# Performance work log

Hardware: AMD Instinct MI355X
Metric: run time of the kernel (lower is better)

The kernel has to match this reference:

```python
import jax, jax.numpy as jnp
import numpy as np

N_NODES = 100000
N_EDGES = 1600000
IN_F = 64
HIDDEN = [64, 64, 32]


def _glorot(key, shape):
    limit = float(np.sqrt(6.0 / (shape[0] + shape[1])))
    return jax.random.uniform(key, shape, jnp.float32, -limit, limit)


def setup_inputs() -> dict:
    key = jax.random.key(0)
    ks = jax.random.split(key, 5)
    x = jax.random.normal(ks[0], (N_NODES, IN_F), jnp.float32)
    edge_index = jax.random.randint(ks[1], (2, N_EDGES), 0, N_NODES, jnp.int64)
    dims = [IN_F] + HIDDEN
    params = {}
    for i in range(len(HIDDEN)):
        params[f"W{i+1}"] = _glorot(ks[2 + i], (dims[i], dims[i + 1]))
        params[f"b{i+1}"] = jnp.zeros((dims[i + 1],), jnp.float32)
    return {"x": x, "edge_index": edge_index, **params}


def _gcn_layer(x, src, dst, norm, W, b, n):
    # PyG GCNConv: linear transform, then normalized scatter-sum aggregation, then bias
    h = x @ W                                  # [N, out]
    msg = norm[:, None] * h[src]               # gather + edge scaling, [E+N, out]
    out = jax.ops.segment_sum(msg, dst, num_segments=n)
    return out + b


def reference(x, edge_index, W1, b1, W2, b2, W3, b3):
    n = x.shape[0]
    # add self-loops (GCNConv default add_self_loops=True)
    loops = jnp.arange(n, dtype=edge_index.dtype)
    src = jnp.concatenate([edge_index[0], loops])
    dst = jnp.concatenate([edge_index[1], loops])
    # symmetric normalization: deg over destination (col), norm = d^-1/2[src]*d^-1/2[dst]
    deg = jax.ops.segment_sum(jnp.ones_like(src, x.dtype), dst, num_segments=n)
    dinv = jnp.where(deg > 0, jax.lax.rsqrt(deg), 0.0)
    norm = dinv[src] * dinv[dst]
    h = jax.nn.relu(_gcn_layer(x, src, dst, norm, W1, b1, n))
    h = jax.nn.relu(_gcn_layer(h, src, dst, norm, W2, b2, n))
    return _gcn_layer(h, src, dst, norm, W3, b3, n)
```

## Files before the change

kernel.cpp:

```cpp
#include <hip/hip_runtime.h>
#include <hip/hip_bf16.h>


#define BLOCK 256
#define NBUCKET 512
#define CHUNK 4096
#define SLOT 4608
#define MAX_NPB 256

typedef float f32x4 __attribute__((ext_vector_type(4)));
typedef short bf16x8 __attribute__((ext_vector_type(8)));

__device__ __forceinline__ unsigned int bf16r(float f) {
  unsigned int u = __float_as_uint(f);
  u += 0x7fffu + ((u >> 16) & 1u);
  return u >> 16;
}

__device__ __forceinline__ void bsplit(float v, unsigned int& h,
                                       unsigned int& l) {
  h = bf16r(v);
  float r = v - __uint_as_float(h << 16);
  l = bf16r(r);
}

__device__ __forceinline__ void acc_bf8(float4& lo, float4& hi, uint4 u) {
  lo.x += __uint_as_float(u.x << 16);
  lo.y += __uint_as_float(u.x & 0xffff0000u);
  lo.z += __uint_as_float(u.y << 16);
  lo.w += __uint_as_float(u.y & 0xffff0000u);
  hi.x += __uint_as_float(u.z << 16);
  hi.y += __uint_as_float(u.z & 0xffff0000u);
  hi.z += __uint_as_float(u.w << 16);
  hi.w += __uint_as_float(u.w & 0xffff0000u);
}


__global__ __launch_bounds__(BLOCK) void binning_kernel(
    const int* __restrict__ src, const int* __restrict__ dst,
    int* __restrict__ bcursor, int* __restrict__ binned, int e, int npb) {
  __shared__ int h[NBUCKET];
  __shared__ int base[NBUCKET];
  for (int i = threadIdx.x; i < NBUCKET; i += BLOCK) h[i] = 0;
  __syncthreads();
  const int cbase = blockIdx.x * CHUNK;
#pragma unroll
  for (int k = 0; k < CHUNK; k += BLOCK * 4) {
    int i = cbase + k + threadIdx.x * 4;
    if (i + 3 < e) {
      int4 d4 = *(const int4*)(dst + i);
      atomicAdd(&h[d4.x / npb], 1);
      atomicAdd(&h[d4.y / npb], 1);
      atomicAdd(&h[d4.z / npb], 1);
      atomicAdd(&h[d4.w / npb], 1);
    } else {
      for (int t = 0; t < 4; ++t)
        if (i + t < e) atomicAdd(&h[dst[i + t] / npb], 1);
    }
  }
  __syncthreads();
  for (int i = threadIdx.x; i < NBUCKET; i += BLOCK) {
    int c = h[i];
    base[i] = c ? atomicAdd(&bcursor[i], c) : 0;
    h[i] = 0;
  }
  __syncthreads();
#pragma unroll
  for (int k = 0; k < CHUNK; k += BLOCK * 4) {
    int i = cbase + k + threadIdx.x * 4;
    if (i + 3 < e) {
      int4 d4 = *(const int4*)(dst + i);
      int4 s4 = *(const int4*)(src + i);
      int b0 = d4.x / npb, b1 = d4.y / npb, b2 = d4.z / npb, b3 = d4.w / npb;
      int o0 = atomicAdd(&h[b0], 1);
      int o1 = atomicAdd(&h[b1], 1);
      int o2 = atomicAdd(&h[b2], 1);
      int o3 = atomicAdd(&h[b3], 1);
      binned[b0 * SLOT + base[b0] + o0] = s4.x | ((d4.x - b0 * npb) << 17);
      binned[b1 * SLOT + base[b1] + o1] = s4.y | ((d4.y - b1 * npb) << 17);
      binned[b2 * SLOT + base[b2] + o2] = s4.z | ((d4.z - b2 * npb) << 17);
      binned[b3 * SLOT + base[b3] + o3] = s4.w | ((d4.w - b3 * npb) << 17);
    } else {
      for (int t = 0; t < 4; ++t) {
        if (i + t < e) {
          int d = dst[i + t];
          int bkt = d / npb;
          int lofs = atomicAdd(&h[bkt], 1);
          binned[bkt * SLOT + base[bkt] + lofs] =
              src[i + t] | ((d - bkt * npb) << 17);
        }
      }
    }
  }
}

__global__ __launch_bounds__(BLOCK) void bucket_build(
    const int* __restrict__ binned, const int* __restrict__ bcursor,
    int* __restrict__ offs, int* __restrict__ cnt, float* __restrict__ dinv,
    int* __restrict__ csr_src, int n, int npb) {
  __shared__ int nhist[MAX_NPB];
  __shared__ int noff[MAX_NPB];
  __shared__ int lcsr[SLOT];
  __shared__ int ptot_sh;
  const int b = blockIdx.x;
  const int node_base = b * npb;
  const int nodes = min(npb, n - node_base);
  if (nodes <= 0) return;
  const int ebase = b * SLOT;
  const int ecnt = bcursor[b];
  for (int i = threadIdx.x; i < npb; i += BLOCK) nhist[i] = 0;
  __syncthreads();
  for (int i = threadIdx.x; i < ecnt; i += BLOCK)
    atomicAdd(&nhist[binned[ebase + i] >> 17], 1);
  __syncthreads();
  if (threadIdx.x < 64) {
    const int lane = threadIdx.x;
    const int bi = lane * 4;
    int v0 = (bi + 0 < nodes) ? nhist[bi + 0] : 0;
    int v1 = (bi + 1 < nodes) ? nhist[bi + 1] : 0;
    int v2 = (bi + 2 < nodes) ? nhist[bi + 2] : 0;
    int v3 = (bi + 3 < nodes) ? nhist[bi + 3] : 0;
    int p0 = (v0 + 3) & ~3;
    int p1 = (v1 + 3) & ~3;
    int p2 = (v2 + 3) & ~3;
    int p3 = (v3 + 3) & ~3;
    int tsum = p0 + p1 + p2 + p3;
    int s = tsum;
#pragma unroll
    for (int o = 1; o < 64; o <<= 1) {
      int u = __shfl_up(s, o, 64);
      if (lane >= o) s += u;
    }
    int texcl = s - tsum;
    if (bi + 0 < nodes) noff[bi + 0] = texcl;
    if (bi + 1 < nodes) noff[bi + 1] = texcl + p0;
    if (bi + 2 < nodes) noff[bi + 2] = texcl + p0 + p1;
    if (bi + 3 < nodes) noff[bi + 3] = texcl + p0 + p1 + p2;
    if (lane == 63) ptot_sh = s;
  }
  __syncthreads();
  const int ptot = min(ptot_sh, SLOT);
  for (int i = threadIdx.x; i < nodes; i += BLOCK) {
    int c = nhist[i];
    offs[node_base + i] = ebase + noff[i];
    cnt[node_base + i] = c;
    dinv[node_base + i] = rsqrtf((float)(c + 1));
  }
  for (int i = threadIdx.x; i < ptot; i += BLOCK) lcsr[i] = n;
  __syncthreads();
  for (int i = threadIdx.x; i < ecnt; i += BLOCK) {
    int v = binned[ebase + i];
    int pos = atomicAdd(&noff[v >> 17], 1);
    lcsr[pos] = v & 0x1ffff;
  }
  __syncthreads();
  for (int i = threadIdx.x; i < ptot; i += BLOCK)
    csr_src[ebase + i] = lcsr[i];
}

__global__ __launch_bounds__(BLOCK) void wprep_kernel(
    const float* __restrict__ W1, const float* __restrict__ W2,
    const float* __restrict__ W3, unsigned short* __restrict__ Wt) {
  int t = blockIdx.x * BLOCK + threadIdx.x;
  float v;
  int hi_off, lo_off;
  if (t < 4096) {
    int nn = t >> 6, k = t & 63;
    v = W1[k * 64 + nn];
    hi_off = t;
    lo_off = 4096 + t;
  } else if (t < 8192) {
    int i = t - 4096;
    int nn = i >> 6, k = i & 63;
    v = W2[k * 64 + nn];
    hi_off = 8192 + i;
    lo_off = 12288 + i;
  } else {
    int i = t - 8192;
    if (i >= 2048) return;
    int nn = i >> 6, k = i & 63;
    v = W3[k * 32 + nn];
    hi_off = 16384 + i;
    lo_off = 18432 + i;
  }
  unsigned int h, l;
  bsplit(v, h, l);
  Wt[hi_off] = (unsigned short)h;
  Wt[lo_off] = (unsigned short)l;
}


__global__ __launch_bounds__(BLOCK) void gemm1_kernel(
    const float* __restrict__ x, const unsigned short* __restrict__ Wt,
    const float* __restrict__ dinv, unsigned short* __restrict__ hbf, int n) {
  __shared__ unsigned short Ahi[16][72];
  __shared__ unsigned short Alo[16][72];
  __shared__ float dvs[16];
  if (blockIdx.x == 0 && threadIdx.x < 8)
    *(uint4*)(hbf + (size_t)n * 64 + threadIdx.x * 8) =
        make_uint4(0u, 0u, 0u, 0u);
  const int r16 = threadIdx.x >> 4;
  const int c4 = (threadIdx.x & 15) * 4;
  const int node = blockIdx.x * 16 + r16;
  const int wv = threadIdx.x >> 6;
  const int fr = threadIdx.x & 15;
  const int fq = (threadIdx.x >> 4) & 3;
  const unsigned short* wb = Wt + ((wv * 16 + fr) * 64) + fq * 8;
  bf16x8 bh0 = *(const bf16x8*)(wb);
  bf16x8 bh1 = *(const bf16x8*)(wb + 32);
  bf16x8 bl0 = *(const bf16x8*)(wb + 4096);
  bf16x8 bl1 = *(const bf16x8*)(wb + 4096 + 32);
  uint2 ph = make_uint2(0u, 0u), pl = make_uint2(0u, 0u);
  if (node < n) {
    f32x4 xv =
        __builtin_nontemporal_load((const f32x4*)(x + (size_t)node * 64 + c4));
    unsigned int h0, l0, h1, l1, h2, l2, h3, l3;
    bsplit(xv.x, h0, l0);
    bsplit(xv.y, h1, l1);
    bsplit(xv.z, h2, l2);
    bsplit(xv.w, h3, l3);
    ph = make_uint2(h0 | (h1 << 16), h2 | (h3 << 16));
    pl = make_uint2(l0 | (l1 << 16), l2 | (l3 << 16));
  }
  *(uint2*)(&Ahi[r16][c4]) = ph;
  *(uint2*)(&Alo[r16][c4]) = pl;
  if ((threadIdx.x & 15) == 0) dvs[r16] = (node < n) ? dinv[node] : 0.f;
  __syncthreads();
  bf16x8 ah0 = *(const bf16x8*)(&Ahi[fr][fq * 8]);
  bf16x8 ah1 = *(const bf16x8*)(&Ahi[fr][fq * 8 + 32]);
  bf16x8 aL0 = *(const bf16x8*)(&Alo[fr][fq * 8]);
  bf16x8 aL1 = *(const bf16x8*)(&Alo[fr][fq * 8 + 32]);
  f32x4 acc = {0.f, 0.f, 0.f, 0.f};
  acc = __builtin_amdgcn_mfma_f32_16x16x32_bf16(ah0, bh0, acc, 0, 0, 0);
  acc = __builtin_amdgcn_mfma_f32_16x16x32_bf16(aL0, bh0, acc, 0, 0, 0);
  acc = __builtin_amdgcn_mfma_f32_16x16x32_bf16(ah0, bl0, acc, 0, 0, 0);
  acc = __builtin_amdgcn_mfma_f32_16x16x32_bf16(ah1, bh1, acc, 0, 0, 0);
  acc = __builtin_amdgcn_mfma_f32_16x16x32_bf16(aL1, bh1, acc, 0, 0, 0);
  acc = __builtin_amdgcn_mfma_f32_16x16x32_bf16(ah1, bl1, acc, 0, 0, 0);
  const int col = wv * 16 + fr;
#pragma unroll
  for (int j = 0; j < 4; ++j) {
    int row = fq * 4 + j;
    int nd = blockIdx.x * 16 + row;
    if (nd < n)
      hbf[(size_t)nd * 64 + col] = (unsigned short)bf16r(dvs[row] * acc[j]);
  }
}

__global__ __launch_bounds__(BLOCK) void fused_agg_gemm64(
    const unsigned short* __restrict__ hin, const int* __restrict__ csr_src,
    const int* __restrict__ offs, const int* __restrict__ cnt,
    const float* __restrict__ dinv, const float* __restrict__ bias,
    const unsigned short* __restrict__ Wt, unsigned short* __restrict__ hout,
    int n) {
  __shared__ unsigned short Ahi[16][72];
  __shared__ unsigned short Alo[16][72];
  __shared__ float dvs[16];
  if (blockIdx.x == 0 && threadIdx.x < 8)
    *(uint4*)(hout + (size_t)n * 64 + threadIdx.x * 8) =
        make_uint4(0u, 0u, 0u, 0u);
  const int g = threadIdx.x >> 4;
  const int lane16 = threadIdx.x & 15;
  const int colgrp = lane16 & 7;
  const int half = lane16 >> 3;
  const int c8 = colgrp * 8;
  const int node = blockIdx.x * 16 + g;
  const bool valid = node < n;
  float dnode = 0.f;
  uint4 qh = make_uint4(0u, 0u, 0u, 0u), ql = make_uint4(0u, 0u, 0u, 0u);
  const char* hbase = (const char*)hin + c8 * 2;
  if (valid) {
    const int start = offs[node];
    const int cn = cnt[node];
    const int* cp = csr_src + start;
    float4 l0 = make_float4(0.f, 0.f, 0.f, 0.f), h0 = l0;
    float4 l1 = l0, h1 = l0, l2 = l0, h2 = l0, l3 = l0, h3 = l0;
    if (half == 0)
      acc_bf8(l0, h0, *(const uint4*)(hbase + ((unsigned)node << 7)));
    int j = half * 4;
    for (; j + 8 < cn; j += 16) {
      int4 sv0 = *(const int4*)(cp + j);
      int4 sv1 = *(const int4*)(cp + j + 8);
      uint4 u0 = *(const uint4*)(hbase + ((unsigned)sv0.x << 7));
      uint4 u1 = *(const uint4*)(hbase + ((unsigned)sv0.y << 7));
      uint4 u2 = *(const uint4*)(hbase + ((unsigned)sv0.z << 7));
      uint4 u3 = *(const uint4*)(hbase + ((unsigned)sv0.w << 7));
      uint4 u4 = *(const uint4*)(hbase + ((unsigned)sv1.x << 7));
      uint4 u5 = *(const uint4*)(hbase + ((unsigned)sv1.y << 7));
      uint4 u6 = *(const uint4*)(hbase + ((unsigned)sv1.z << 7));
      uint4 u7 = *(const uint4*)(hbase + ((unsigned)sv1.w << 7));
      acc_bf8(l0, h0, u0);
      acc_bf8(l1, h1, u1);
      acc_bf8(l2, h2, u2);
      acc_bf8(l3, h3, u3);
      acc_bf8(l0, h0, u4);
      acc_bf8(l1, h1, u5);
      acc_bf8(l2, h2, u6);
      acc_bf8(l3, h3, u7);
    }
    if (j < cn) {
      int4 sv = *(const int4*)(cp + j);
      uint4 u0 = *(const uint4*)(hbase + ((unsigned)sv.x << 7));
      uint4 u1 = *(const uint4*)(hbase + ((unsigned)sv.y << 7));
      uint4 u2 = *(const uint4*)(hbase + ((unsigned)sv.z << 7));
      uint4 u3 = *(const uint4*)(hbase + ((unsigned)sv.w << 7));
      acc_bf8(l0, h0, u0);
      acc_bf8(l1, h1, u1);
      acc_bf8(l2, h2, u2);
      acc_bf8(l3, h3, u3);
    }
    float4 alo = make_float4((l0.x + l1.x) + (l2.x + l3.x),
                             (l0.y + l1.y) + (l2.y + l3.y),
                             (l0.z + l1.z) + (l2.z + l3.z),
                             (l0.w + l1.w) + (l2.w + l3.w));
    float4 ahi = make_float4((h0.x + h1.x) + (h2.x + h3.x),
                             (h0.y + h1.y) + (h2.y + h3.y),
                             (h0.z + h1.z) + (h2.z + h3.z),
                             (h0.w + h1.w) + (h2.w + h3.w));
    alo.x += __shfl_xor(alo.x, 8); alo.y += __shfl_xor(alo.y, 8);
    alo.z += __shfl_xor(alo.z, 8); alo.w += __shfl_xor(alo.w, 8);
    ahi.x += __shfl_xor(ahi.x, 8); ahi.y += __shfl_xor(ahi.y, 8);
    ahi.z += __shfl_xor(ahi.z, 8); ahi.w += __shfl_xor(ahi.w, 8);
    dnode = dinv[node];
    if (half == 0) {
      float4 b4l = *(const float4*)(bias + c8);
      float4 b4h = *(const float4*)(bias + c8 + 4);
      float v0 = fmaxf(fmaf(dnode, alo.x, b4l.x), 0.f);
      float v1 = fmaxf(fmaf(dnode, alo.y, b4l.y), 0.f);
      float v2 = fmaxf(fmaf(dnode, alo.z, b4l.z), 0.f);
      float v3 = fmaxf(fmaf(dnode, alo.w, b4l.w), 0.f);
      float v4 = fmaxf(fmaf(dnode, ahi.x, b4h.x), 0.f);
      float v5 = fmaxf(fmaf(dnode, ahi.y, b4h.y), 0.f);
      float v6 = fmaxf(fmaf(dnode, ahi.z, b4h.z), 0.f);
      float v7 = fmaxf(fmaf(dnode, ahi.w, b4h.w), 0.f);
      unsigned int h0u, l0u, h1u, l1u, h2u, l2u, h3u, l3u;
      unsigned int h4u, l4u, h5u, l5u, h6u, l6u, h7u, l7u;
      bsplit(v0, h0u, l0u); bsplit(v1, h1u, l1u);
      bsplit(v2, h2u, l2u); bsplit(v3, h3u, l3u);
      bsplit(v4, h4u, l4u); bsplit(v5, h5u, l5u);
      bsplit(v6, h6u, l6u); bsplit(v7, h7u, l7u);
      qh = make_uint4(h0u | (h1u << 16), h2u | (h3u << 16),
                      h4u | (h5u << 16), h6u | (h7u << 16));
      ql = make_uint4(l0u | (l1u << 16), l2u | (l3u << 16),
                      l4u | (l5u << 16), l6u | (l7u << 16));
    }
  }
  if (half == 0) {
    *(uint4*)(&Ahi[g][c8]) = qh;
    *(uint4*)(&Alo[g][c8]) = ql;
    if (lane16 == 0) dvs[g] = dnode;
  }
  const int wv = threadIdx.x >> 6;
  const int fr = threadIdx.x & 15;
  const int fq = (threadIdx.x >> 4) & 3;
  const unsigned short* wb = Wt + ((wv * 16 + fr) * 64) + fq * 8;
  bf16x8 bh0 = *(const bf16x8*)(wb);
  bf16x8 bh1 = *(const bf16x8*)(wb + 32);
  bf16x8 bl0 = *(const bf16x8*)(wb + 4096);
  bf16x8 bl1 = *(const bf16x8*)(wb + 4096 + 32);
  __syncthreads();
  bf16x8 ah0 = *(const bf16x8*)(&Ahi[fr][fq * 8]);
  bf16x8 ah1 = *(const bf16x8*)(&Ahi[fr][fq * 8 + 32]);
  bf16x8 aL0 = *(const bf16x8*)(&Alo[fr][fq * 8]);
  bf16x8 aL1 = *(const bf16x8*)(&Alo[fr][fq * 8 + 32]);
  f32x4 acc = {0.f, 0.f, 0.f, 0.f};
  acc = __builtin_amdgcn_mfma_f32_16x16x32_bf16(ah0, bh0, acc, 0, 0, 0);
  acc = __builtin_amdgcn_mfma_f32_16x16x32_bf16(aL0, bh0, acc, 0, 0, 0);
  acc = __builtin_amdgcn_mfma_f32_16x16x32_bf16(ah0, bl0, acc, 0, 0, 0);
  acc = __builtin_amdgcn_mfma_f32_16x16x32_bf16(ah1, bh1, acc, 0, 0, 0);
  acc = __builtin_amdgcn_mfma_f32_16x16x32_bf16(aL1, bh1, acc, 0, 0, 0);
  acc = __builtin_amdgcn_mfma_f32_16x16x32_bf16(ah1, bl1, acc, 0, 0, 0);
  const int col = wv * 16 + fr;
#pragma unroll
  for (int j = 0; j < 4; ++j) {
    int row = fq * 4 + j;
    int nd = blockIdx.x * 16 + row;
    if (nd < n)
      hout[(size_t)nd * 64 + col] = (unsigned short)bf16r(dvs[row] * acc[j]);
  }
}

__global__ __launch_bounds__(BLOCK) void fused_agg_gemm32(
    const unsigned short* __restrict__ hin, const int* __restrict__ csr_src,
    const int* __restrict__ offs, const int* __restrict__ cnt,
    const float* __restrict__ dinv, const float* __restrict__ bias,
    const unsigned short* __restrict__ Wt, unsigned short* __restrict__ hout,
    int n) {
  __shared__ unsigned short Ahi[32][72];
  __shared__ unsigned short Alo[32][72];
  __shared__ float dvs[32];
  if (blockIdx.x == 0 && threadIdx.x < 4)
    *(uint4*)(hout + (size_t)n * 32 + threadIdx.x * 8) =
        make_uint4(0u, 0u, 0u, 0u);
  const int g = threadIdx.x >> 3;
  const int lane8 = threadIdx.x & 7;
  const int c8 = lane8 * 8;
  const int node = blockIdx.x * 32 + g;
  const bool valid = node < n;
  float dnode = 0.f;
  uint4 qh = make_uint4(0u, 0u, 0u, 0u), ql = make_uint4(0u, 0u, 0u, 0u);
  const char* hbase = (const char*)hin + c8 * 2;
  if (valid) {
    const int start = offs[node];
    const int cn = cnt[node];
    const int* cp = csr_src + start;
    float4 l0 = make_float4(0.f, 0.f, 0.f, 0.f), h0 = l0;
    float4 l1 = l0, h1 = l0, l2 = l0, h2 = l0, l3 = l0, h3 = l0;
    acc_bf8(l0, h0, *(const uint4*)(hbase + ((unsigned)node << 7)));
    int j = 0;
    for (; j + 4 < cn; j += 8) {
      int4 sv0 = *(const int4*)(cp + j);
      int4 sv1 = *(const int4*)(cp + j + 4);
      uint4 u0 = *(const uint4*)(hbase + ((unsigned)sv0.x << 7));
      uint4 u1 = *(const uint4*)(hbase + ((unsigned)sv0.y << 7));
      uint4 u2 = *(const uint4*)(hbase + ((unsigned)sv0.z << 7));
      uint4 u3 = *(const uint4*)(hbase + ((unsigned)sv0.w << 7));
      uint4 u4 = *(const uint4*)(hbase + ((unsigned)sv1.x << 7));
      uint4 u5 = *(const uint4*)(hbase + ((unsigned)sv1.y << 7));
      uint4 u6 = *(const uint4*)(hbase + ((unsigned)sv1.z << 7));
      uint4 u7 = *(const uint4*)(hbase + ((unsigned)sv1.w << 7));
      acc_bf8(l0, h0, u0);
      acc_bf8(l1, h1, u1);
      acc_bf8(l2, h2, u2);
      acc_bf8(l3, h3, u3);
      acc_bf8(l0, h0, u4);
      acc_bf8(l1, h1, u5);
      acc_bf8(l2, h2, u6);
      acc_bf8(l3, h3, u7);
    }
    if (j < cn) {
      int4 sv = *(const int4*)(cp + j);
      uint4 u0 = *(const uint4*)(hbase + ((unsigned)sv.x << 7));
      uint4 u1 = *(const uint4*)(hbase + ((unsigned)sv.y << 7));
      uint4 u2 = *(const uint4*)(hbase + ((unsigned)sv.z << 7));
      uint4 u3 = *(const uint4*)(hbase + ((unsigned)sv.w << 7));
      acc_bf8(l0, h0, u0);
      acc_bf8(l1, h1, u1);
      acc_bf8(l2, h2, u2);
      acc_bf8(l3, h3, u3);
    }
    float4 alo = make_float4((l0.x + l1.x) + (l2.x + l3.x),
                             (l0.y + l1.y) + (l2.y + l3.y),
                             (l0.z + l1.z) + (l2.z + l3.z),
                             (l0.w + l1.w) + (l2.w + l3.w));
    float4 ahi = make_float4((h0.x + h1.x) + (h2.x + h3.x),
                             (h0.y + h1.y) + (h2.y + h3.y),
                             (h0.z + h1.z) + (h2.z + h3.z),
                             (h0.w + h1.w) + (h2.w + h3.w));
    dnode = dinv[node];
    float4 b4l = *(const float4*)(bias + c8);
    float4 b4h = *(const float4*)(bias + c8 + 4);
    float v0 = fmaxf(fmaf(dnode, alo.x, b4l.x), 0.f);
    float v1 = fmaxf(fmaf(dnode, alo.y, b4l.y), 0.f);
    float v2 = fmaxf(fmaf(dnode, alo.z, b4l.z), 0.f);
    float v3 = fmaxf(fmaf(dnode, alo.w, b4l.w), 0.f);
    float v4 = fmaxf(fmaf(dnode, ahi.x, b4h.x), 0.f);
    float v5 = fmaxf(fmaf(dnode, ahi.y, b4h.y), 0.f);
    float v6 = fmaxf(fmaf(dnode, ahi.z, b4h.z), 0.f);
    float v7 = fmaxf(fmaf(dnode, ahi.w, b4h.w), 0.f);
    unsigned int h0u, l0u, h1u, l1u, h2u, l2u, h3u, l3u;
    unsigned int h4u, l4u, h5u, l5u, h6u, l6u, h7u, l7u;
    bsplit(v0, h0u, l0u); bsplit(v1, h1u, l1u);
    bsplit(v2, h2u, l2u); bsplit(v3, h3u, l3u);
    bsplit(v4, h4u, l4u); bsplit(v5, h5u, l5u);
    bsplit(v6, h6u, l6u); bsplit(v7, h7u, l7u);
    qh = make_uint4(h0u | (h1u << 16), h2u | (h3u << 16),
                    h4u | (h5u << 16), h6u | (h7u << 16));
    ql = make_uint4(l0u | (l1u << 16), l2u | (l3u << 16),
                    l4u | (l5u << 16), l6u | (l7u << 16));
  }
  *(uint4*)(&Ahi[g][c8]) = qh;
  *(uint4*)(&Alo[g][c8]) = ql;
  if (lane8 == 0) dvs[g] = dnode;
  const int wv = threadIdx.x >> 6;
  const int mt = wv >> 1;
  const int nt = wv & 1;
  const int fr = threadIdx.x & 15;
  const int fq = (threadIdx.x >> 4) & 3;
  const unsigned short* wb = Wt + ((nt * 16 + fr) * 64) + fq * 8;
  bf16x8 bh0 = *(const bf16x8*)(wb);
  bf16x8 bh1 = *(const bf16x8*)(wb + 32);
  bf16x8 bl0 = *(const bf16x8*)(wb + 2048);
  bf16x8 bl1 = *(const bf16x8*)(wb + 2048 + 32);
  __syncthreads();
  bf16x8 ah0 = *(const bf16x8*)(&Ahi[mt * 16 + fr][fq * 8]);
  bf16x8 ah1 = *(const bf16x8*)(&Ahi[mt * 16 + fr][fq * 8 + 32]);
  bf16x8 aL0 = *(const bf16x8*)(&Alo[mt * 16 + fr][fq * 8]);
  bf16x8 aL1 = *(const bf16x8*)(&Alo[mt * 16 + fr][fq * 8 + 32]);
  f32x4 acc = {0.f, 0.f, 0.f, 0.f};
  acc = __builtin_amdgcn_mfma_f32_16x16x32_bf16(ah0, bh0, acc, 0, 0, 0);
  acc = __builtin_amdgcn_mfma_f32_16x16x32_bf16(aL0, bh0, acc, 0, 0, 0);
  acc = __builtin_amdgcn_mfma_f32_16x16x32_bf16(ah0, bl0, acc, 0, 0, 0);
  acc = __builtin_amdgcn_mfma_f32_16x16x32_bf16(ah1, bh1, acc, 0, 0, 0);
  acc = __builtin_amdgcn_mfma_f32_16x16x32_bf16(aL1, bh1, acc, 0, 0, 0);
  acc = __builtin_amdgcn_mfma_f32_16x16x32_bf16(ah1, bl1, acc, 0, 0, 0);
  const int col = nt * 16 + fr;
#pragma unroll
  for (int j = 0; j < 4; ++j) {
    int row = mt * 16 + fq * 4 + j;
    int nd = blockIdx.x * 32 + row;
    if (nd < n)
      hout[(size_t)nd * 32 + col] = (unsigned short)bf16r(dvs[row] * acc[j]);
  }
}

__global__ __launch_bounds__(BLOCK) void agg3_kernel(
    const unsigned short* __restrict__ hbf, const int* __restrict__ csr_src,
    const int* __restrict__ offs, const int* __restrict__ cnt,
    const float* __restrict__ dinv, const float* __restrict__ bias,
    float* __restrict__ out, int n) {
  constexpr int F = 32;
  const int node = blockIdx.x * 64 + (int)(threadIdx.x >> 2);
  const int c8 = (threadIdx.x & 3) * 8;
  if (node >= n) return;
  const int start = offs[node];
  const int cn = cnt[node];
  const int* cp = csr_src + start;
  const char* hbase = (const char*)hbf + c8 * 2;
  float4 l0 = make_float4(0.f, 0.f, 0.f, 0.f), h0 = l0;
  float4 l1 = l0, h1 = l0, l2 = l0, h2 = l0, l3 = l0, h3 = l0;
  acc_bf8(l0, h0, *(const uint4*)(hbase + ((unsigned)node << 6)));
  for (int j = 0; j < cn; j += 4) {
    int4 sv = *(const int4*)(cp + j);
    uint4 u0 = *(const uint4*)(hbase + ((unsigned)sv.x << 6));
    uint4 u1 = *(const uint4*)(hbase + ((unsigned)sv.y << 6));
    uint4 u2 = *(const uint4*)(hbase + ((unsigned)sv.z << 6));
    uint4 u3 = *(const uint4*)(hbase + ((unsigned)sv.w << 6));
    acc_bf8(l0, h0, u0);
    acc_bf8(l1, h1, u1);
    acc_bf8(l2, h2, u2);
    acc_bf8(l3, h3, u3);
  }
  float4 alo = make_float4((l0.x + l1.x) + (l2.x + l3.x),
                           (l0.y + l1.y) + (l2.y + l3.y),
                           (l0.z + l1.z) + (l2.z + l3.z),
                           (l0.w + l1.w) + (l2.w + l3.w));
  float4 ahi = make_float4((h0.x + h1.x) + (h2.x + h3.x),
                           (h0.y + h1.y) + (h2.y + h3.y),
                           (h0.z + h1.z) + (h2.z + h3.z),
                           (h0.w + h1.w) + (h2.w + h3.w));
  float d = dinv[node];
  float4 blo = *(const float4*)(bias + c8);
  float4 bhi = *(const float4*)(bias + c8 + 4);
  f32x4 vlo = {fmaf(d, alo.x, blo.x), fmaf(d, alo.y, blo.y),
               fmaf(d, alo.z, blo.z), fmaf(d, alo.w, blo.w)};
  f32x4 vhi = {fmaf(d, ahi.x, bhi.x), fmaf(d, ahi.y, bhi.y),
               fmaf(d, ahi.z, bhi.z), fmaf(d, ahi.w, bhi.w)};
  float* op = out + (size_t)node * F + c8;
  __builtin_nontemporal_store(vlo, (f32x4*)op);
  __builtin_nontemporal_store(vhi, (f32x4*)(op + 4));
}

static inline size_t align_up(size_t v, size_t a) { return (v + a - 1) & ~(a - 1); }

extern "C" void kernel_launch(void* const* d_in, const int* in_sizes, int n_in,
                              void* d_out, int out_size, void* d_ws, size_t ws_size,
                              hipStream_t stream) {
  const float* x = (const float*)d_in[0];
  const int* edge_index = (const int*)d_in[1];
  const float* W1 = (const float*)d_in[2];
  const float* b1 = (const float*)d_in[3];
  const float* W2 = (const float*)d_in[4];
  const float* b2 = (const float*)d_in[5];
  const float* W3 = (const float*)d_in[6];
  const float* b3 = (const float*)d_in[7];
  float* out = (float*)d_out;

  const int n = in_sizes[0] / 64;
  const int e = in_sizes[1] / 2;
  const int* e_src = edge_index;
  const int* e_dst = edge_index + e;
  const int npb = (n + NBUCKET - 1) / NBUCKET;

  char* ws = (char*)d_ws;
  size_t off = 0;
  int* bcursor = (int*)(ws + off); off = align_up(off + NBUCKET * 4, 512);
  int* offs    = (int*)(ws + off); off = align_up(off + (size_t)n * 4, 512);
  int* cnt     = (int*)(ws + off); off = align_up(off + (size_t)n * 4, 512);
  float* dinv  = (float*)(ws + off); off = align_up(off + (size_t)n * 4, 512);
  int* binned  = (int*)(ws + off); off = align_up(off + (size_t)NBUCKET * SLOT * 4, 512);
  int* csr_src = (int*)(ws + off); off = align_up(off + (size_t)NBUCKET * SLOT * 4, 512);
  unsigned short* hbuf_a = (unsigned short*)(ws + off);
  off = align_up(off + (size_t)(n + 1) * 64 * 2, 512);
  unsigned short* hbuf_b = (unsigned short*)(ws + off);
  off = align_up(off + (size_t)(n + 1) * 64 * 2, 512);
  unsigned short* Wt = (unsigned short*)(ws + off);
  off = align_up(off + (size_t)20480 * 2, 512);
  (void)ws_size;

  unsigned short* Wt1 = Wt;
  unsigned short* Wt2 = Wt + 8192;
  unsigned short* Wt3 = Wt + 16384;

  const int gC = (e + CHUNK - 1) / CHUNK;

  hipMemsetAsync(bcursor, 0, NBUCKET * 4, stream);
  wprep_kernel<<<40, BLOCK, 0, stream>>>(W1, W2, W3, Wt);
  binning_kernel<<<gC, BLOCK, 0, stream>>>(e_src, e_dst, bcursor, binned, e, npb);
  bucket_build<<<NBUCKET, BLOCK, 0, stream>>>(binned, bcursor, offs, cnt, dinv,
                                              csr_src, n, npb);

  gemm1_kernel<<<(n + 15) / 16, BLOCK, 0, stream>>>(x, Wt1, dinv, hbuf_a, n);
  fused_agg_gemm64<<<(n + 15) / 16, BLOCK, 0, stream>>>(
      hbuf_a, csr_src, offs, cnt, dinv, b1, Wt2, hbuf_b, n);
  fused_agg_gemm32<<<(n + 31) / 32, BLOCK, 0, stream>>>(
      hbuf_b, csr_src, offs, cnt, dinv, b2, Wt3, hbuf_a, n);
  agg3_kernel<<<(n + 63) / 64, BLOCK, 0, stream>>>(hbuf_a, csr_src, offs, cnt,
                                                   dinv, b3, out, n);
}
```

Before: 237.3 us.

## Fold weight prep into binning, scatter CSR directly, unroll agg3 loop

The weight bf16 split/transpose moves into the binning kernel, which removes one kernel launch. bucket_build now writes CSR entries straight to global memory with per-node padding instead of staging them in a shared buffer, which cuts shared memory and two sync phases. The final aggregation loop is unrolled to 8 neighbours per iteration to keep more gathers in flight. The trade-off is scattered global writes in bucket_build and a small amount of extra work in binning blocks.

```diff
diff --git a/kernel.cpp b/kernel.cpp
--- a/kernel.cpp
+++ b/kernel.cpp
@@ -38,7 +38,47 @@
 
 __global__ __launch_bounds__(BLOCK) void binning_kernel(
     const int* __restrict__ src, const int* __restrict__ dst,
-    int* __restrict__ bcursor, int* __restrict__ binned, int e, int npb) {
+    int* __restrict__ bcursor, int* __restrict__ binned,
+    const float* __restrict__ W1, const float* __restrict__ W2,
+    const float* __restrict__ W3, unsigned short* __restrict__ Wt, int e,
+    int npb) {
+  {
+    int t = blockIdx.x * BLOCK + threadIdx.x;
+    if (t < 20480) {
+      float v;
+      int hi_off, lo_off;
+      if (t < 4096) {
+        int nn = t >> 6, k = t & 63;
+        v = W1[k * 64 + nn];
+        hi_off = t;
+        lo_off = 4096 + t;
+      } else if (t < 8192) {
+        int i = t - 4096;
+        int nn = i >> 6, k = i & 63;
+        v = W2[k * 64 + nn];
+        hi_off = 8192 + i;
+        lo_off = 12288 + i;
+      } else {
+        int i = t - 8192;
+        if (i < 2048) {
+          int nn = i >> 6, k = i & 63;
+          v = W3[k * 32 + nn];
+          hi_off = 16384 + i;
+          lo_off = 18432 + i;
+        } else {
+          hi_off = -1;
+          lo_off = -1;
+          v = 0.f;
+        }
+      }
+      if (hi_off >= 0) {
+        unsigned int h, l;
+        bsplit(v, h, l);
+        Wt[hi_off] = (unsigned short)h;
+        Wt[lo_off] = (unsigned short)l;
+      }
+    }
+  }
   __shared__ int h[NBUCKET];
   __shared__ int base[NBUCKET];
   for (int i = threadIdx.x; i < NBUCKET; i += BLOCK) h[i] = 0;
@@ -99,9 +139,8 @@
     int* __restrict__ offs, int* __restrict__ cnt, float* __restrict__ dinv,
     int* __restrict__ csr_src, int n, int npb) {
   __shared__ int nhist[MAX_NPB];
+  __shared__ int nbase[MAX_NPB];
   __shared__ int noff[MAX_NPB];
-  __shared__ int lcsr[SLOT];
-  __shared__ int ptot_sh;
   const int b = blockIdx.x;
   const int node_base = b * npb;
   const int nodes = min(npb, n - node_base);
@@ -132,61 +171,38 @@
       if (lane >= o) s += u;
     }
     int texcl = s - tsum;
-    if (bi + 0 < nodes) noff[bi + 0] = texcl;
-    if (bi + 1 < nodes) noff[bi + 1] = texcl + p0;
-    if (bi + 2 < nodes) noff[bi + 2] = texcl + p0 + p1;
-    if (bi + 3 < nodes) noff[bi + 3] = texcl + p0 + p1 + p2;
-    if (lane == 63) ptot_sh = s;
-  }
-  __syncthreads();
-  const int ptot = min(ptot_sh, SLOT);
+    if (bi + 0 < nodes) { nbase[bi + 0] = texcl; noff[bi + 0] = texcl; }
+    if (bi + 1 < nodes) {
+      nbase[bi + 1] = texcl + p0;
+      noff[bi + 1] = texcl + p0;
+    }
+    if (bi + 2 < nodes) {
+      nbase[bi + 2] = texcl + p0 + p1;
+      noff[bi + 2] = texcl + p0 + p1;
+    }
+    if (bi + 3 < nodes) {
+      nbase[bi + 3] = texcl + p0 + p1 + p2;
+      noff[bi + 3] = texcl + p0 + p1 + p2;
+    }
+  }
+  __syncthreads();
   for (int i = threadIdx.x; i < nodes; i += BLOCK) {
     int c = nhist[i];
-    offs[node_base + i] = ebase + noff[i];
+    offs[node_base + i] = ebase + nbase[i];
     cnt[node_base + i] = c;
     dinv[node_base + i] = rsqrtf((float)(c + 1));
   }
-  for (int i = threadIdx.x; i < ptot; i += BLOCK) lcsr[i] = n;
-  __syncthreads();
   for (int i = threadIdx.x; i < ecnt; i += BLOCK) {
     int v = binned[ebase + i];
     int pos = atomicAdd(&noff[v >> 17], 1);
-    lcsr[pos] = v & 0x1ffff;
-  }
-  __syncthreads();
-  for (int i = threadIdx.x; i < ptot; i += BLOCK)
-    csr_src[ebase + i] = lcsr[i];
-}
-
-__global__ __launch_bounds__(BLOCK) void wprep_kernel(
-    const float* __restrict__ W1, const float* __restrict__ W2,
-    const float* __restrict__ W3, unsigned short* __restrict__ Wt) {
-  int t = blockIdx.x * BLOCK + threadIdx.x;
-  float v;
-  int hi_off, lo_off;
-  if (t < 4096) {
-    int nn = t >> 6, k = t & 63;
-    v = W1[k * 64 + nn];
-    hi_off = t;
-    lo_off = 4096 + t;
-  } else if (t < 8192) {
-    int i = t - 4096;
-    int nn = i >> 6, k = i & 63;
-    v = W2[k * 64 + nn];
-    hi_off = 8192 + i;
-    lo_off = 12288 + i;
-  } else {
-    int i = t - 8192;
-    if (i >= 2048) return;
-    int nn = i >> 6, k = i & 63;
-    v = W3[k * 32 + nn];
-    hi_off = 16384 + i;
-    lo_off = 18432 + i;
-  }
-  unsigned int h, l;
-  bsplit(v, h, l);
-  Wt[hi_off] = (unsigned short)h;
-  Wt[lo_off] = (unsigned short)l;
+    csr_src[ebase + pos] = v & 0x1ffff;
+  }
+  for (int i = threadIdx.x; i < nodes; i += BLOCK) {
+    int c = nhist[i];
+    int basei = ebase + nbase[i] + c;
+    int pads = ((c + 3) & ~3) - c;
+    for (int k = 0; k < pads; ++k) csr_src[basei + k] = n;
+  }
 }
 
 
@@ -520,7 +536,28 @@
   float4 l0 = make_float4(0.f, 0.f, 0.f, 0.f), h0 = l0;
   float4 l1 = l0, h1 = l0, l2 = l0, h2 = l0, l3 = l0, h3 = l0;
   acc_bf8(l0, h0, *(const uint4*)(hbase + ((unsigned)node << 6)));
-  for (int j = 0; j < cn; j += 4) {
+  int j = 0;
+  for (; j + 4 < cn; j += 8) {
+    int4 sv0 = *(const int4*)(cp + j);
+    int4 sv1 = *(const int4*)(cp + j + 4);
+    uint4 u0 = *(const uint4*)(hbase + ((unsigned)sv0.x << 6));
+    uint4 u1 = *(const uint4*)(hbase + ((unsigned)sv0.y << 6));
+    uint4 u2 = *(const uint4*)(hbase + ((unsigned)sv0.z << 6));
+    uint4 u3 = *(const uint4*)(hbase + ((unsigned)sv0.w << 6));
+    uint4 u4 = *(const uint4*)(hbase + ((unsigned)sv1.x << 6));
+    uint4 u5 = *(const uint4*)(hbase + ((unsigned)sv1.y << 6));
+    uint4 u6 = *(const uint4*)(hbase + ((unsigned)sv1.z << 6));
+    uint4 u7 = *(const uint4*)(hbase + ((unsigned)sv1.w << 6));
+    acc_bf8(l0, h0, u0);
+    acc_bf8(l1, h1, u1);
+    acc_bf8(l2, h2, u2);
+    acc_bf8(l3, h3, u3);
+    acc_bf8(l0, h0, u4);
+    acc_bf8(l1, h1, u5);
+    acc_bf8(l2, h2, u6);
+    acc_bf8(l3, h3, u7);
+  }
+  if (j < cn) {
     int4 sv = *(const int4*)(cp + j);
     uint4 u0 = *(const uint4*)(hbase + ((unsigned)sv.x << 6));
     uint4 u1 = *(const uint4*)(hbase + ((unsigned)sv.y << 6));
@@ -595,8 +632,8 @@
   const int gC = (e + CHUNK - 1) / CHUNK;
 
   hipMemsetAsync(bcursor, 0, NBUCKET * 4, stream);
-  wprep_kernel<<<40, BLOCK, 0, stream>>>(W1, W2, W3, Wt);
-  binning_kernel<<<gC, BLOCK, 0, stream>>>(e_src, e_dst, bcursor, binned, e, npb);
+  binning_kernel<<<gC, BLOCK, 0, stream>>>(e_src, e_dst, bcursor, binned, W1,
+                                           W2, W3, Wt, e, npb);
   bucket_build<<<NBUCKET, BLOCK, 0, stream>>>(binned, bcursor, offs, cnt, dinv,
                                               csr_src, n, npb);
 
```

Measured after the change: 236.0 us. About the same (-0.5%).
